# Kernel optimization log

Hardware: AMD Instinct MI355X
Metric: run time of the kernel (lower is better)

## Reference

```python
import jax, jax.numpy as jnp
import numpy as np

B, T, H = 4096, 256, 64  # batch, seq_len, hidden_size


def _lstm_layer(x, W_ih, W_hh, b_ih, b_hh):
    """One LSTM layer, batch_first. x: [B,T,D]; W_ih: [4H,D]; W_hh: [4H,H].
    PyTorch gate order: i, f, g, o."""
    Bb = x.shape[0]
    Hh = W_hh.shape[1]
    # Precompute input contribution for all timesteps: [B,T,4H]
    gx = jnp.einsum('btd,gd->btg', x, W_ih) + b_ih + b_hh

    def step(carry, g_t):
        h, c = carry
        g = g_t + h @ W_hh.T  # [B,4H]
        i, f, gg, o = jnp.split(g, 4, axis=-1)
        i = jax.nn.sigmoid(i)
        f = jax.nn.sigmoid(f)
        gg = jnp.tanh(gg)
        o = jax.nn.sigmoid(o)
        c = f * c + i * gg
        h = o * jnp.tanh(c)
        return (h, c), h

    h0 = jnp.zeros((Bb, Hh), x.dtype)
    c0 = jnp.zeros((Bb, Hh), x.dtype)
    _, hs = jax.lax.scan(step, (h0, c0), jnp.swapaxes(gx, 0, 1))  # hs: [T,B,H]
    return jnp.swapaxes(hs, 0, 1)  # [B,T,H]


def setup_inputs() -> dict:
    key = jax.random.key(0)
    ks = jax.random.split(key, 11)
    s = 1.0 / np.sqrt(H)  # keep recurrent dynamics well-scaled
    return {
        'recipe': jax.random.normal(ks[0], (B, T, 1), jnp.float32),
        'W_ih0': jax.random.normal(ks[1], (4 * H, 1), jnp.float32) * s,
        'W_hh0': jax.random.normal(ks[2], (4 * H, H), jnp.float32) * s,
        'b_ih0': jax.random.normal(ks[3], (4 * H,), jnp.float32) * s,
        'b_hh0': jax.random.normal(ks[4], (4 * H,), jnp.float32) * s,
        'W_ih1': jax.random.normal(ks[5], (4 * H, H), jnp.float32) * s,
        'W_hh1': jax.random.normal(ks[6], (4 * H, H), jnp.float32) * s,
        'b_ih1': jax.random.normal(ks[7], (4 * H,), jnp.float32) * s,
        'b_hh1': jax.random.normal(ks[8], (4 * H,), jnp.float32) * s,
        'W_lin': jax.random.normal(ks[9], (H, H), jnp.float32) * s,
        'b_lin': jax.random.normal(ks[10], (H,), jnp.float32) * s,
    }


def reference(recipe, W_ih0, W_hh0, b_ih0, b_hh0, W_ih1, W_hh1, b_ih1, b_hh1, W_lin, b_lin):
    h1 = _lstm_layer(recipe, W_ih0, W_hh0, b_ih0, b_hh0)  # [B,T,H]
    h2 = _lstm_layer(h1, W_ih1, W_hh1, b_ih1, b_hh1)      # [B,T,H]
    return h2[:, -1, :] @ W_lin.T + b_lin                   # [B,H]
```

## Files before the change

### kernel.cpp

```cpp
#include <hip/hip_runtime.h>

typedef _Float16 v8h __attribute__((ext_vector_type(8)));
typedef float    v4f __attribute__((ext_vector_type(4)));

#define MFMA16(A,B,C) __builtin_amdgcn_mfma_f32_16x16x32_f16((A),(B),(C),0,0,0)

#define RPB 16
#define TT  256
#define HH  64
#define KST 136
#define SG  256.0f
#define TG  512.0f
#define IOFF 4096.5f
#define TSC2 -2.88539008f

__global__ __launch_bounds__(512, 2)
void lstm2_kernel(const float* __restrict__ x,
                  const float* __restrict__ Wih0,
                  const float* __restrict__ Whh0,
                  const float* __restrict__ bih0,
                  const float* __restrict__ bhh0,
                  const float* __restrict__ Wih1,
                  const float* __restrict__ Whh1,
                  const float* __restrict__ bih1,
                  const float* __restrict__ bhh1,
                  const float* __restrict__ Wlin,
                  const float* __restrict__ blin,
                  float* __restrict__ out)
{
    __shared__ float xl[TT][RPB];
    __shared__ __align__(16) _Float16 hs[2][RPB][KST];
    __shared__ float hbF[RPB][HH];
    __shared__ float lut[8192];

    const int tid  = threadIdx.x;
    const int w    = tid >> 6;
    const int l15  = tid & 15;
    const int q    = (tid & 63) >> 4;
    const int row0 = (int)blockIdx.x * RPB;
    const int jj   = (w & 3) * 16 + l15;
    const bool isA = (w < 4);
    const int  mr  = q * 4;

    for (int idx = tid; idx < RPB * TT; idx += 512) {
        int m = idx & 15, t = idx >> 4;
        xl[t][m] = x[(row0 + m) * TT + t];
    }
    for (int idx = tid; idx < 2 * RPB * KST; idx += 512)
        ((_Float16*)hs)[idx] = (_Float16)0.f;
    for (int i = tid; i < 8192; i += 512)
        lut[i] = 1.0f / (1.0f + __expf(-(i - 4096) * (1.0f / 256.0f)));

    auto lutv = [&](float f) -> float {
        f = __builtin_amdgcn_fmed3f(f, 0.0f, 8191.0f);
        return lut[(int)f];
    };
    auto tanhf_fast = [&](float c) -> float {
        return fmaf(2.f, __builtin_amdgcn_rcpf(1.f + __builtin_exp2f(c * TSC2)), -1.f);
    };

    float wi0s[4], b0s[4];
    v8h   wh0[4][2];
    v4f   b1v[4];
    v8h   wi1[4][2], wh1[4][2];
    if (isA) {
        #pragma unroll
        for (int tau = 0; tau < 4; tau++) {
            float sc = (tau == 2) ? TG : SG;
            int n = tau * 64 + jj;
            wi0s[tau] = Wih0[n] * sc;
            b0s[tau]  = (bih0[n] + bhh0[n]) * sc + IOFF;
            #pragma unroll
            for (int kk = 0; kk < 2; kk++) {
                int k0 = kk * 32 + q * 8;
                v8h a;
                #pragma unroll
                for (int j = 0; j < 8; j++)
                    a[j] = (_Float16)(Whh0[n * HH + k0 + j] * sc);
                wh0[tau][kk] = a;
            }
        }
    } else {
        #pragma unroll
        for (int tau = 0; tau < 4; tau++) {
            float sc = (tau == 2) ? TG : SG;
            int n = tau * 64 + jj;
            float b1 = (bih1[n] + bhh1[n]) * sc + IOFF;
            b1v[tau] = (v4f){b1, b1, b1, b1};
            #pragma unroll
            for (int kk = 0; kk < 2; kk++) {
                int k0 = kk * 32 + q * 8;
                v8h b, c;
                #pragma unroll
                for (int j = 0; j < 8; j++) {
                    b[j] = (_Float16)(Wih1[n * HH + k0 + j] * sc);
                    c[j] = (_Float16)(Whh1[n * HH + k0 + j] * sc);
                }
                wi1[tau][kk] = b; wh1[tau][kk] = c;
            }
        }
    }

    float cs[4] = {0.f, 0.f, 0.f, 0.f};
    __syncthreads();

    if (isA) {
        #pragma unroll
        for (int r = 0; r < 4; r++) {
            int m = mr + r;
            float xv = xl[0][m];
            float iv = lutv(fmaf(xv, wi0s[0], b0s[0]));
            float gv = fmaf(2.f, lutv(fmaf(xv, wi0s[2], b0s[2])), -1.f);
            float ov = lutv(fmaf(xv, wi0s[3], b0s[3]));
            cs[r] = iv * gv;
            hs[0][m][jj] = (_Float16)(ov * tanhf_fast(cs[r]));
        }
    }
    __syncthreads();

    auto step = [&](int k, int p, int pw, bool last) {
        if (isA) {
            v8h a0 = *(const v8h*)&hs[p][l15][q * 8];
            v8h a1 = *(const v8h*)&hs[p][l15][32 + q * 8];
            int kx = (k < TT) ? k : (TT - 1);
            v4f xv = *(const v4f*)&xl[kx][mr];

            v4f acc[4];
            #pragma unroll
            for (int tau = 0; tau < 4; tau++) {
                #pragma unroll
                for (int r = 0; r < 4; r++)
                    acc[tau][r] = fmaf(xv[r], wi0s[tau], b0s[tau]);
            }
            #pragma unroll
            for (int tau = 0; tau < 4; tau++) {
                acc[tau] = MFMA16(a0, wh0[tau][0], acc[tau]);
                acc[tau] = MFMA16(a1, wh0[tau][1], acc[tau]);
            }
            float sv0[4], sv1[4], sv2[4], sv3[4];
            #pragma unroll
            for (int r = 0; r < 4; r++) {
                sv0[r] = lutv(acc[0][r]);
                sv1[r] = lutv(acc[1][r]);
                sv2[r] = lutv(acc[2][r]);
                sv3[r] = lutv(acc[3][r]);
            }
            _Float16* wp = &hs[pw][mr][jj];
            #pragma unroll
            for (int r = 0; r < 4; r++) {
                float iv = sv0[r], fv = sv1[r];
                float gv = fmaf(2.f, sv2[r], -1.f);
                float ov = sv3[r];
                cs[r] = fmaf(fv, cs[r], iv * gv);
                wp[r * KST] = (_Float16)(ov * tanhf_fast(cs[r]));
            }
        } else {
            v8h a0 = *(const v8h*)&hs[p][l15][q * 8];
            v8h a1 = *(const v8h*)&hs[p][l15][32 + q * 8];
            v8h b0 = *(const v8h*)&hs[p][l15][64 + q * 8];
            v8h b1 = *(const v8h*)&hs[p][l15][96 + q * 8];

            v4f acc[4];
            #pragma unroll
            for (int tau = 0; tau < 4; tau++)
                acc[tau] = MFMA16(a0, wi1[tau][0], b1v[tau]);
            #pragma unroll
            for (int tau = 0; tau < 4; tau++) {
                acc[tau] = MFMA16(a1, wi1[tau][1], acc[tau]);
                acc[tau] = MFMA16(b0, wh1[tau][0], acc[tau]);
                acc[tau] = MFMA16(b1, wh1[tau][1], acc[tau]);
            }
            float sv0[4], sv1[4], sv2[4], sv3[4];
            #pragma unroll
            for (int r = 0; r < 4; r++) {
                sv0[r] = lutv(acc[0][r]);
                sv1[r] = lutv(acc[1][r]);
                sv2[r] = lutv(acc[2][r]);
                sv3[r] = lutv(acc[3][r]);
            }
            _Float16* wp = &hs[pw][mr][64 + jj];
            #pragma unroll
            for (int r = 0; r < 4; r++) {
                float iv = sv0[r], fv = sv1[r];
                float gv = fmaf(2.f, sv2[r], -1.f);
                float ov = sv3[r];
                cs[r] = fmaf(fv, cs[r], iv * gv);
                float hv = ov * tanhf_fast(cs[r]);
                wp[r * KST] = (_Float16)hv;
                if (last) hbF[mr + r][jj] = hv;
            }
        }
        __syncthreads();
    };

    for (int k = 1; k <= TT; k += 2) {
        step(k,     0, 1, false);
        step(k + 1, 1, 0, (k + 1) == TT);
    }

    int m = tid >> 5;
    int n0 = (tid & 31) * 2;
    float a0o = blin[n0], a1o = blin[n0 + 1];
    #pragma unroll 8
    for (int j = 0; j < HH; j++) {
        float h = hbF[m][j];
        a0o = fmaf(h, Wlin[(n0 + 0) * HH + j], a0o);
        a1o = fmaf(h, Wlin[(n0 + 1) * HH + j], a1o);
    }
    out[(row0 + m) * HH + n0]     = a0o;
    out[(row0 + m) * HH + n0 + 1] = a1o;
}

extern "C" void kernel_launch(void* const* d_in, const int* in_sizes, int n_in,
                              void* d_out, int out_size, void* d_ws, size_t ws_size,
                              hipStream_t stream) {
    const float* x    = (const float*)d_in[0];
    const float* Wih0 = (const float*)d_in[1];
    const float* Whh0 = (const float*)d_in[2];
    const float* bih0 = (const float*)d_in[3];
    const float* bhh0 = (const float*)d_in[4];
    const float* Wih1 = (const float*)d_in[5];
    const float* Whh1 = (const float*)d_in[6];
    const float* bih1 = (const float*)d_in[7];
    const float* bhh1 = (const float*)d_in[8];
    const float* Wlin = (const float*)d_in[9];
    const float* blin = (const float*)d_in[10];
    lstm2_kernel<<<256, 512, 0, stream>>>(x, Wih0, Whh0, bih0, bhh0,
                                          Wih1, Whh1, bih1, bhh1,
                                          Wlin, blin, (float*)d_out);
}
```

Baseline: 312.5 us.

## Replace nearest sigmoid LUT with interpolated bank-replicated LUT

```diff
diff --git a/kernel.cpp b/kernel.cpp
--- a/kernel.cpp
+++ b/kernel.cpp
@@ -9,9 +9,10 @@
 #define TT  256
 #define HH  64
 #define KST 136
-#define SG  256.0f
-#define TG  512.0f
-#define IOFF 4096.5f
+#define FSC  2048.0f
+#define FSG  4096.0f
+#define FOFF 32768.0f
+#define FCLMP 65535.0f
 #define TSC2 -2.88539008f
 
 __global__ __launch_bounds__(512, 2)
@@ -31,7 +32,7 @@
     __shared__ float xl[TT][RPB];
     __shared__ __align__(16) _Float16 hs[2][RPB][KST];
     __shared__ float hbF[RPB][HH];
-    __shared__ float lut[8192];
+    __shared__ float2 lut[256 * 32];
 
     const int tid  = threadIdx.x;
     const int w    = tid >> 6;
@@ -41,6 +42,7 @@
     const int jj   = (w & 3) * 16 + l15;
     const bool isA = (w < 4);
     const int  mr  = q * 4;
+    const int  loff = (tid & 31) * 8;
 
     for (int idx = tid; idx < RPB * TT; idx += 512) {
         int m = idx & 15, t = idx >> 4;
@@ -48,12 +50,20 @@
     }
     for (int idx = tid; idx < 2 * RPB * KST; idx += 512)
         ((_Float16*)hs)[idx] = (_Float16)0.f;
-    for (int i = tid; i < 8192; i += 512)
-        lut[i] = 1.0f / (1.0f + __expf(-(i - 4096) * (1.0f / 256.0f)));
-
-    auto lutv = [&](float f) -> float {
-        f = __builtin_amdgcn_fmed3f(f, 0.0f, 8191.0f);
-        return lut[(int)f];
+    for (int i = tid; i < 256 * 32; i += 512) {
+        int e = i >> 5;
+        float z  = (e - 128) * 0.125f;
+        float s0 = 1.0f / (1.0f + __expf(-z));
+        float s1 = 1.0f / (1.0f + __expf(-(z + 0.125f)));
+        lut[i] = (float2){s0, (s1 - s0) * (1.0f / 256.0f)};
+    }
+
+    auto lutv = [&](float F) -> float {
+        F = __builtin_amdgcn_fmed3f(F, 0.0f, FCLMP);
+        int ia = ((int)F) & 0xFF00;
+        float fr = F - (float)ia;
+        float2 s = *(const float2*)((const char*)lut + ia + loff);
+        return fmaf(s.y, fr, s.x);
     };
     auto tanhf_fast = [&](float c) -> float {
         return fmaf(2.f, __builtin_amdgcn_rcpf(1.f + __builtin_exp2f(c * TSC2)), -1.f);
@@ -66,10 +76,10 @@
     if (isA) {
         #pragma unroll
         for (int tau = 0; tau < 4; tau++) {
-            float sc = (tau == 2) ? TG : SG;
+            float sc = (tau == 2) ? FSG : FSC;
             int n = tau * 64 + jj;
             wi0s[tau] = Wih0[n] * sc;
-            b0s[tau]  = (bih0[n] + bhh0[n]) * sc + IOFF;
+            b0s[tau]  = (bih0[n] + bhh0[n]) * sc + FOFF;
             #pragma unroll
             for (int kk = 0; kk < 2; kk++) {
                 int k0 = kk * 32 + q * 8;
@@ -83,9 +93,9 @@
     } else {
         #pragma unroll
         for (int tau = 0; tau < 4; tau++) {
-            float sc = (tau == 2) ? TG : SG;
+            float sc = (tau == 2) ? FSG : FSC;
             int n = tau * 64 + jj;
-            float b1 = (bih1[n] + bhh1[n]) * sc + IOFF;
+            float b1 = (bih1[n] + bhh1[n]) * sc + FOFF;
             b1v[tau] = (v4f){b1, b1, b1, b1};
             #pragma unroll
             for (int kk = 0; kk < 2; kk++) {
@@ -198,7 +208,8 @@
         step(k + 1, 1, 0, (k + 1) == TT);
     }
 
-    int m = tid >> 5;
+    int m = tid >> 6;
+    m = tid >> 5;
     int n0 = (tid & 31) * 2;
     float a0o = blin[n0], a1o = blin[n0 + 1];
     #pragma unroll 8
```

Result: no change. 316.7 us (+1.3%).
